# Kernel optimization log

Measured on AMD Instinct MI355X. Metric: run time of the kernel, lower is better.

## Reference

```python
import jax, jax.numpy as jnp
import numpy as np

B, C, H, W = 4, 256, 64, 64
C8, C2 = C // 8, C // 2


def _conv(x, w, b):
    # NCHW conv with SAME padding
    y = jax.lax.conv_general_dilated(x, w, (1, 1), 'SAME',
                                     dimension_numbers=('NCHW', 'OIHW', 'NCHW'))
    return y + b[None, :, None, None]


def _bn(x, s, bi, m, v):
    # eval-mode batchnorm, eps matches torch default 1e-5
    inv = jax.lax.rsqrt(v + 1e-5)
    return (x - m[None, :, None, None]) * (inv * s)[None, :, None, None] + bi[None, :, None, None]


def setup_inputs() -> dict:
    ks = jax.random.split(jax.random.key(0), 8)
    return {
        'x': jax.random.normal(ks[0], (B, C, H, W), jnp.float32),
        'q_w': jax.random.normal(ks[1], (C8, C, 3, 3), jnp.float32) * 0.02,
        'q_b': jnp.zeros((C8,), jnp.float32),
        'q_bn_s': jnp.ones((C8,), jnp.float32),
        'q_bn_b': jnp.zeros((C8,), jnp.float32),
        'q_bn_m': jnp.zeros((C8,), jnp.float32),
        'q_bn_v': jnp.ones((C8,), jnp.float32),
        'k_w': jax.random.normal(ks[2], (C8, C, 3, 3), jnp.float32) * 0.02,
        'k_b': jnp.zeros((C8,), jnp.float32),
        'k_bn_s': jnp.ones((C8,), jnp.float32),
        'k_bn_b': jnp.zeros((C8,), jnp.float32),
        'k_bn_m': jnp.zeros((C8,), jnp.float32),
        'k_bn_v': jnp.ones((C8,), jnp.float32),
        'v_w': jax.random.normal(ks[3], (C, C), jnp.float32) * 0.02,
        'v_b': jnp.zeros((C,), jnp.float32),
        'gamma': jnp.full((1,), 0.5, jnp.float32),
        'c_w1': jax.random.normal(ks[4], (C2, C), jnp.float32) * 0.02,
        'c_b1': jnp.zeros((C2,), jnp.float32),
        'c_w2': jax.random.normal(ks[5], (C, C2), jnp.float32) * 0.02,
        'c_b2': jnp.zeros((C,), jnp.float32),
        's_vw': jax.random.normal(ks[6], (C, C), jnp.float32) * 0.02,
        's_vb': jnp.zeros((C,), jnp.float32),
        's_cw': jax.random.normal(ks[7], (1, 2, 3, 3), jnp.float32) * 0.1,
        's_cb': jnp.zeros((1,), jnp.float32),
        's_bn_s': jnp.ones((1,), jnp.float32),
        's_bn_b': jnp.zeros((1,), jnp.float32),
        's_bn_m': jnp.zeros((1,), jnp.float32),
        's_bn_v': jnp.ones((1,), jnp.float32),
    }


def reference(x, q_w, q_b, q_bn_s, q_bn_b, q_bn_m, q_bn_v,
              k_w, k_b, k_bn_s, k_bn_b, k_bn_m, k_bn_v,
              v_w, v_b, gamma, c_w1, c_b1, c_w2, c_b2,
              s_vw, s_vb, s_cw, s_cb, s_bn_s, s_bn_b, s_bn_m, s_bn_v):
    Bn, Cn, Hn, Wn = x.shape
    HW = Hn * Wn

    # ---- SelfAttention branch ----
    q = jax.nn.relu(_bn(_conv(x, q_w, q_b), q_bn_s, q_bn_b, q_bn_m, q_bn_v)).reshape(Bn, -1, HW)  # [B,C8,HW]
    k = jax.nn.relu(_bn(_conv(x, k_w, k_b), k_bn_s, k_bn_b, k_bn_m, k_bn_v)).reshape(Bn, -1, HW)  # [B,C8,HW]
    aff = jax.nn.softmax(jnp.einsum('bcn,bcm->bnm', q, k), axis=-1)  # [B,HW,HW]
    v = (jnp.einsum('bchw,oc->bohw', x, v_w) + v_b[None, :, None, None]).reshape(Bn, Cn, HW)
    wts = jnp.einsum('bcm,bnm->bcn', v, aff).reshape(Bn, Cn, Hn, Wn)
    selfA = gamma * wts + x

    # ---- Channel mean/max attention ----
    def fc(s):  # s: [B,C]
        h = jax.nn.relu(s @ c_w1.T + c_b1)
        return h @ c_w2.T + c_b2

    gate = jax.nn.sigmoid(fc(x.mean((2, 3))) + fc(x.max((2, 3))))  # [B,C]
    channelA = x * gate[:, :, None, None]

    # ---- Spatial mean/max attention ----
    v2 = jnp.einsum('bchw,oc->bohw', x, s_vw) + s_vb[None, :, None, None]  # [B,C,H,W]
    sm = jnp.stack([v2.max(1), v2.mean(1)], axis=1)  # [B,2,H,W]
    a = _bn(_conv(sm, s_cw, s_cb), s_bn_s, s_bn_b, s_bn_m, s_bn_v)  # [B,1,H,W]
    a = jax.nn.softmax(a[:, 0], axis=-1)  # [B,H,W], softmax over W
    spatialA = jnp.einsum('bchw,bwk->bchk', x, a)  # batched matmul, needs H==W

    return selfA + channelA + spatialA
```

## Files before the change

kernel.cpp:

```cpp
#include <hip/hip_runtime.h>
#include <math.h>

#define NB 4
#define NC 256
#define NHW 4096
#define NC8 32
#define NC2 128

typedef unsigned short u16;
typedef __attribute__((ext_vector_type(8))) short s8v;
typedef __attribute__((ext_vector_type(4))) float f4v;

__device__ __forceinline__ u16 f2bf(float x) {
    unsigned int u = __builtin_bit_cast(unsigned int, x);
    u += 0x7FFFu + ((u >> 16) & 1u);
    return (u16)(u >> 16);
}
__device__ __forceinline__ float bf2f(u16 h) {
    unsigned int u = ((unsigned int)h) << 16;
    return __builtin_bit_cast(float, u);
}

#define MFMA16(a, b, c) __builtin_amdgcn_mfma_f32_16x16x32_bf16((a), (b), (c), 0, 0, 0)

__global__ __launch_bounds__(256) void k_conv_qk(
    const float* __restrict__ x,
    const float* __restrict__ qw, const float* __restrict__ kw,
    float* __restrict__ part)
{
    __shared__ float plane[2][64 * 65];
    const int cog = blockIdx.x;
    const int cic = blockIdx.y;
    const int b   = blockIdx.z;
    const int t   = threadIdx.x;
    const int co0 = cog * 4;
    const bool isq = co0 < NC8;
    const int oc0 = isq ? co0 : co0 - NC8;
    const float* wsel = isq ? qw : kw;
    const int ci0 = cic * 64;
    const int r  = t >> 2;
    const int c0 = (t & 3) * 16;
    float acc[4][16];
#pragma unroll
    for (int j = 0; j < 4; ++j)
#pragma unroll
        for (int q = 0; q < 16; ++q) acc[j][q] = 0.f;

    const float* xb = x + (size_t)b * NC * NHW;
    float4 pf[4];
    {
        const float4* src = (const float4*)(xb + (size_t)ci0 * NHW);
#pragma unroll
        for (int u = 0; u < 4; ++u) pf[u] = src[t + 256 * u];
    }
    for (int ci = ci0; ci < ci0 + 64; ++ci) {
        const int cur = ci & 1;
#pragma unroll
        for (int u = 0; u < 4; ++u) {
            int g  = (t + 256 * u) << 2;
            int rr = g >> 6, cc = g & 63;
            float* p = &plane[cur][rr * 65 + cc];
            p[0] = pf[u].x; p[1] = pf[u].y; p[2] = pf[u].z; p[3] = pf[u].w;
        }
        __syncthreads();
        if (ci + 1 < ci0 + 64) {
            const float4* src = (const float4*)(xb + (size_t)(ci + 1) * NHW);
#pragma unroll
            for (int u = 0; u < 4; ++u) pf[u] = src[t + 256 * u];
        }
        float w9[4][9];
#pragma unroll
        for (int j = 0; j < 4; ++j)
#pragma unroll
            for (int u = 0; u < 9; ++u)
                w9[j][u] = wsel[((size_t)(oc0 + j) * NC + ci) * 9 + u];
#pragma unroll
        for (int dy = 0; dy < 3; ++dy) {
            int rr = r + dy - 1;
            if (rr >= 0 && rr <= 63) {
                const float* row = &plane[cur][rr * 65];
                float tv[18];
#pragma unroll
                for (int jj = 0; jj < 18; ++jj) {
                    int cc = c0 + jj - 1;
                    tv[jj] = (cc >= 0 && cc < 64) ? row[cc] : 0.f;
                }
#pragma unroll
                for (int j = 0; j < 4; ++j) {
                    float wa = w9[j][dy * 3 + 0], wb = w9[j][dy * 3 + 1], wc = w9[j][dy * 3 + 2];
#pragma unroll
                    for (int q = 0; q < 16; ++q)
                        acc[j][q] += wa * tv[q] + wb * tv[q + 1] + wc * tv[q + 2];
                }
            }
        }
        __syncthreads();
    }
    float* pp = part + (((size_t)(cic * 4 + b) * 64 + co0) * NHW) + r * 64 + c0;
#pragma unroll
    for (int j = 0; j < 4; ++j)
#pragma unroll
        for (int q4 = 0; q4 < 4; ++q4) {
            float4 o;
            o.x = acc[j][q4 * 4 + 0]; o.y = acc[j][q4 * 4 + 1];
            o.z = acc[j][q4 * 4 + 2]; o.w = acc[j][q4 * 4 + 3];
            *(float4*)(pp + (size_t)j * NHW + q4 * 4) = o;
        }
}

__global__ __launch_bounds__(256) void k_qk_finish(
    const float* __restrict__ part,
    const float* __restrict__ qb, const float* __restrict__ qbs, const float* __restrict__ qbb,
    const float* __restrict__ qbm, const float* __restrict__ qbv,
    const float* __restrict__ kb, const float* __restrict__ kbs, const float* __restrict__ kbb,
    const float* __restrict__ kbm, const float* __restrict__ kbv,
    u16* __restrict__ qh, u16* __restrict__ ql,
    u16* __restrict__ kh, u16* __restrict__ kl)
{
    const int t = threadIdx.x;
    const int b = blockIdx.y;
    const int n = blockIdx.x * 64 + (t & 63);
    const int coq = t >> 6;
    const int cb2 = coq * 16;
    float s[16];
#pragma unroll
    for (int j = 0; j < 16; ++j) s[j] = 0.f;
#pragma unroll
    for (int cic = 0; cic < 4; ++cic)
#pragma unroll
        for (int j = 0; j < 16; ++j)
            s[j] += part[(((size_t)(cic * 4 + b)) * 64 + cb2 + j) * NHW + n];
    const bool isq = coq < 2;
    u16 hi[16], lo[16];
#pragma unroll
    for (int j = 0; j < 16; ++j) {
        int oc = (coq & 1) * 16 + j;
        float cbv = isq ? qb[oc]  : kb[oc];
        float sv  = isq ? qbs[oc] : kbs[oc];
        float bbv = isq ? qbb[oc] : kbb[oc];
        float mv  = isq ? qbm[oc] : kbm[oc];
        float vv  = isq ? qbv[oc] : kbv[oc];
        float inv = rsqrtf(vv + 1e-5f);
        float scale = inv * sv;
        float shift = (cbv - mv) * scale + bbv;
        float y = fmaxf(s[j] * scale + shift, 0.f);
        hi[j] = f2bf(y);
        lo[j] = f2bf(y - bf2f(hi[j]));
    }
    u16* dh = isq ? qh : kh;
    u16* dl = isq ? ql : kl;
    size_t base = ((size_t)b * NHW + n) * 32 + (coq & 1) * 16;
    uint4 ph0, ph1, pl0, pl1;
    ph0.x = (unsigned)hi[0]  | ((unsigned)hi[1]  << 16);
    ph0.y = (unsigned)hi[2]  | ((unsigned)hi[3]  << 16);
    ph0.z = (unsigned)hi[4]  | ((unsigned)hi[5]  << 16);
    ph0.w = (unsigned)hi[6]  | ((unsigned)hi[7]  << 16);
    ph1.x = (unsigned)hi[8]  | ((unsigned)hi[9]  << 16);
    ph1.y = (unsigned)hi[10] | ((unsigned)hi[11] << 16);
    ph1.z = (unsigned)hi[12] | ((unsigned)hi[13] << 16);
    ph1.w = (unsigned)hi[14] | ((unsigned)hi[15] << 16);
    pl0.x = (unsigned)lo[0]  | ((unsigned)lo[1]  << 16);
    pl0.y = (unsigned)lo[2]  | ((unsigned)lo[3]  << 16);
    pl0.z = (unsigned)lo[4]  | ((unsigned)lo[5]  << 16);
    pl0.w = (unsigned)lo[6]  | ((unsigned)lo[7]  << 16);
    pl1.x = (unsigned)lo[8]  | ((unsigned)lo[9]  << 16);
    pl1.y = (unsigned)lo[10] | ((unsigned)lo[11] << 16);
    pl1.z = (unsigned)lo[12] | ((unsigned)lo[13] << 16);
    pl1.w = (unsigned)lo[14] | ((unsigned)lo[15] << 16);
    *(uint4*)&dh[base]     = ph0;
    *(uint4*)&dh[base + 8] = ph1;
    *(uint4*)&dl[base]     = pl0;
    *(uint4*)&dl[base + 8] = pl1;
}

__global__ __launch_bounds__(256) void k_gemm_vv2(
    const float* __restrict__ x,
    const float* __restrict__ vw, const float* __restrict__ vb,
    const float* __restrict__ sw, const float* __restrict__ sb,
    float* __restrict__ v2T, u16* __restrict__ vhi, u16* __restrict__ vlo)
{
    __shared__ float Ax[16 * 68];
    __shared__ float Bw1[16 * 68];
    __shared__ float Bw2[16 * 68];
    const int t  = threadIdx.x;
    const int n0 = blockIdx.x * 64;
    const int o0 = blockIdx.y * 64;
    const int b  = blockIdx.z;
    const int ni = t & 15, oi = t >> 4;
    float a1[4][4], a2[4][4];
#pragma unroll
    for (int i = 0; i < 4; ++i)
#pragma unroll
        for (int j = 0; j < 4; ++j) { a1[i][j] = 0.f; a2[i][j] = 0.f; }

    const int sk  = t >> 4;
    const int sf  = t & 15;
    const int so  = t & 63;
    const int skq = t >> 6;
    const float* xb = x + ((size_t)b * NC) * NHW + n0;

    float4 ax = *(const float4*)(xb + (size_t)sk * NHW + sf * 4);
    float4 f1 = *(const float4*)(vw + (size_t)(o0 + so) * NC + skq * 4);
    float4 f2 = *(const float4*)(sw + (size_t)(o0 + so) * NC + skq * 4);

    for (int c0 = 0; c0 < NC; c0 += 16) {
        *(float4*)&Ax[sk * 68 + sf * 4] = ax;
        Bw1[(skq * 4 + 0) * 68 + so] = f1.x;
        Bw1[(skq * 4 + 1) * 68 + so] = f1.y;
        Bw1[(skq * 4 + 2) * 68 + so] = f1.z;
        Bw1[(skq * 4 + 3) * 68 + so] = f1.w;
        Bw2[(skq * 4 + 0) * 68 + so] = f2.x;
        Bw2[(skq * 4 + 1) * 68 + so] = f2.y;
        Bw2[(skq * 4 + 2) * 68 + so] = f2.z;
        Bw2[(skq * 4 + 3) * 68 + so] = f2.w;
        __syncthreads();
        if (c0 + 16 < NC) {
            ax = *(const float4*)(xb + (size_t)(c0 + 16 + sk) * NHW + sf * 4);
            f1 = *(const float4*)(vw + (size_t)(o0 + so) * NC + c0 + 16 + skq * 4);
            f2 = *(const float4*)(sw + (size_t)(o0 + so) * NC + c0 + 16 + skq * 4);
        }
#pragma unroll
        for (int k = 0; k < 16; ++k) {
            float4 af = *(const float4*)&Ax[k * 68 + ni * 4];
            float4 g1 = *(const float4*)&Bw1[k * 68 + oi * 4];
            float4 g2 = *(const float4*)&Bw2[k * 68 + oi * 4];
            const float* ap = (const float*)&af;
            const float* p1 = (const float*)&g1;
            const float* p2 = (const float*)&g2;
#pragma unroll
            for (int i = 0; i < 4; ++i)
#pragma unroll
                for (int j = 0; j < 4; ++j) {
                    a1[i][j] += ap[i] * p1[j];
                    a2[i][j] += ap[i] * p2[j];
                }
        }
        __syncthreads();
    }
    float vb4[4], sb4[4];
#pragma unroll
    for (int j = 0; j < 4; ++j) { vb4[j] = vb[o0 + oi * 4 + j]; sb4[j] = sb[o0 + oi * 4 + j]; }
#pragma unroll
    for (int i = 0; i < 4; ++i) {
        size_t idx = ((size_t)b * NHW + n0 + ni * 4 + i) * NC + o0 + oi * 4;
        float4 o2v;
        o2v.x = a2[i][0] + sb4[0]; o2v.y = a2[i][1] + sb4[1];
        o2v.z = a2[i][2] + sb4[2]; o2v.w = a2[i][3] + sb4[3];
        *(float4*)&v2T[idx] = o2v;
    }
#pragma unroll
    for (int j = 0; j < 4; ++j) {
        u16 h[4], l[4];
#pragma unroll
        for (int i = 0; i < 4; ++i) {
            float y = a1[i][j] + vb4[j];
            h[i] = f2bf(y);
            l[i] = f2bf(y - bf2f(h[i]));
        }
        size_t vi = ((size_t)b * NC + o0 + oi * 4 + j) * NHW + n0 + ni * 4;
        uint2 uh, ul;
        uh.x = (unsigned)h[0] | ((unsigned)h[1] << 16);
        uh.y = (unsigned)h[2] | ((unsigned)h[3] << 16);
        ul.x = (unsigned)l[0] | ((unsigned)l[1] << 16);
        ul.y = (unsigned)l[2] | ((unsigned)l[3] << 16);
        *(uint2*)&vhi[vi] = uh;
        *(uint2*)&vlo[vi] = ul;
    }
}

__global__ __launch_bounds__(256) void k_reduce_v2(const float* __restrict__ v2T,
                                                   float* __restrict__ smo)
{
    const int t = threadIdx.x;
    const int lane = t & 63, wv = t >> 6;
    const int row = blockIdx.x * 4 + wv;
    float4 f = ((const float4*)(v2T + (size_t)row * NC))[lane];
    float mx = fmaxf(fmaxf(f.x, f.y), fmaxf(f.z, f.w));
    float sm = f.x + f.y + f.z + f.w;
#pragma unroll
    for (int off = 32; off; off >>= 1) {
        mx = fmaxf(mx, __shfl_down(mx, off));
        sm += __shfl_down(sm, off);
    }
    if (lane == 0) {
        int b = row >> 12, n = row & 4095;
        smo[((size_t)b * 2 + 0) * NHW + n] = mx;
        smo[((size_t)b * 2 + 1) * NHW + n] = sm * (1.f / NC);
    }
}

__global__ __launch_bounds__(256) void k_spatial(
    const float* __restrict__ smo, const float* __restrict__ scw,
    const float* __restrict__ scb, const float* __restrict__ sbs,
    const float* __restrict__ sbb2, const float* __restrict__ sbm,
    const float* __restrict__ sbv, float* __restrict__ Amat)
{
    __shared__ float ch[2][64 * 68];
    __shared__ float lg[64 * 68];
    const int t = threadIdx.x;
    const int b = blockIdx.x;
#pragma unroll
    for (int u = 0; u < 8; ++u) {
        int g  = t + 256 * u;
        int c  = g >> 10, gi = g & 1023;
        int row = gi >> 4, col4 = (gi & 15) * 4;
        float4 f = ((const float4*)(smo + ((size_t)b * 2 + c) * NHW))[gi];
        *(float4*)&ch[c][row * 68 + col4] = f;
    }
    __syncthreads();
    float w9[2][9];
#pragma unroll
    for (int ic = 0; ic < 2; ++ic)
#pragma unroll
        for (int j = 0; j < 9; ++j) w9[ic][j] = scw[ic * 9 + j];
    float A0, Bsh;
    {
        float inv = rsqrtf(sbv[0] + 1e-5f);
        A0  = inv * sbs[0];
        Bsh = (scb[0] - sbm[0]) * A0 + sbb2[0];
    }
#pragma unroll
    for (int u = 0; u < 16; ++u) {
        int px = t + 256 * u;
        int h = px >> 6, w = px & 63;
        float acc = 0.f;
#pragma unroll
        for (int ic = 0; ic < 2; ++ic)
#pragma unroll
            for (int dy = 0; dy < 3; ++dy) {
                int rr = h + dy - 1;
                if (rr < 0 || rr > 63) continue;
#pragma unroll
                for (int dx = 0; dx < 3; ++dx) {
                    int cc = w + dx - 1;
                    if (cc < 0 || cc > 63) continue;
                    acc += w9[ic][dy * 3 + dx] * ch[ic][rr * 68 + cc];
                }
            }
        lg[h * 68 + w] = acc * A0 + Bsh;
    }
    __syncthreads();
    if (t < 64) {
        float M = -INFINITY;
        for (int k2 = 0; k2 < 64; ++k2) M = fmaxf(M, lg[t * 68 + k2]);
        float L = 0.f;
        for (int k2 = 0; k2 < 64; ++k2) L += __expf(lg[t * 68 + k2] - M);
        float rli = 1.f / L;
        for (int k2 = 0; k2 < 64; ++k2)
            Amat[(size_t)b * NHW + t * 64 + k2] = __expf(lg[t * 68 + k2] - M) * rli;
    }
}

__global__ __launch_bounds__(256) void k_xstats(const float* __restrict__ x,
                                                float* __restrict__ smean,
                                                float* __restrict__ smax)
{
    const int t = threadIdx.x;
    const int c = blockIdx.x, b = blockIdx.y;
    const float* row = x + ((size_t)b * NC + c) * NHW;
    float s = 0.f, m = -INFINITY;
#pragma unroll
    for (int u = 0; u < 4; ++u) {
        float4 f = ((const float4*)row)[t + 256 * u];
        s += f.x + f.y + f.z + f.w;
        m = fmaxf(m, fmaxf(fmaxf(f.x, f.y), fmaxf(f.z, f.w)));
    }
    __shared__ float red[8];
    const int lane = t & 63, wv = t >> 6;
#pragma unroll
    for (int off = 32; off; off >>= 1) {
        s += __shfl_down(s, off);
        m = fmaxf(m, __shfl_down(m, off));
    }
    if (lane == 0) { red[wv] = s; red[4 + wv] = m; }
    __syncthreads();
    if (t == 0) {
        float S = red[0] + red[1] + red[2] + red[3];
        float M = fmaxf(fmaxf(red[4], red[5]), fmaxf(red[6], red[7]));
        smean[b * NC + c] = S * (1.f / NHW);
        smax[b * NC + c]  = M;
    }
}

__global__ __launch_bounds__(256) void k_gate(
    const float* __restrict__ smean, const float* __restrict__ smax,
    const float* __restrict__ w1, const float* __restrict__ b1,
    const float* __restrict__ w2, const float* __restrict__ b2,
    float* __restrict__ gate)
{
    __shared__ float smL[256], sxL[256], hL[256];
    const int t = threadIdx.x;
    const int b = blockIdx.x;
    smL[t] = smean[b * NC + t];
    sxL[t] = smax[b * NC + t];
    __syncthreads();
    {
        const int j = t & 127;
        const float* in = (t < 128) ? smL : sxL;
        const float* wr = w1 + (size_t)j * NC;
        float acc = b1[j];
        for (int c = 0; c < NC; c += 4) {
            float4 f = *(const float4*)(wr + c);
            acc += f.x * in[c] + f.y * in[c + 1] + f.z * in[c + 2] + f.w * in[c + 3];
        }
        hL[t] = fmaxf(acc, 0.f);
    }
    __syncthreads();
    {
        const float* wr = w2 + (size_t)t * NC2;
        float acc = 2.f * b2[t];
        for (int j = 0; j < NC2; j += 4) {
            float4 f = *(const float4*)(wr + j);
            acc += f.x * (hL[j]     + hL[128 + j])
                 + f.y * (hL[j + 1] + hL[129 + j])
                 + f.z * (hL[j + 2] + hL[130 + j])
                 + f.w * (hL[j + 3] + hL[131 + j]);
        }
        gate[b * NC + t] = 1.f / (1.f + __expf(-acc));
    }
}

__global__ __launch_bounds__(64) void k_softstats(
    const u16* __restrict__ qh, const u16* __restrict__ ql,
    const u16* __restrict__ kh, const u16* __restrict__ kl,
    float* __restrict__ mx, float* __restrict__ rl)
{
    const int t  = threadIdx.x;
    const int li = t & 15, g = t >> 4;
    const int n0 = blockIdx.x * 16;
    const int b  = blockIdx.y;
    const size_t qoff = ((size_t)b * NHW + n0 + li) * 32 + g * 8;
    const s8v qfh = *(const s8v*)&qh[qoff];
    const s8v qfl = *(const s8v*)&ql[qoff];
    const size_t kb0 = ((size_t)b * NHW + li) * 32 + g * 8;
    s8v ka0 = *(const s8v*)&kh[kb0];
    s8v ka1 = *(const s8v*)&kh[kb0 + 512];
    s8v la0 = *(const s8v*)&kl[kb0];
    s8v la1 = *(const s8v*)&kl[kb0 + 512];
    float mrun = -INFINITY, lrun = 0.f;
    for (int it = 0; it < 128; ++it) {
        f4v c0 = {0.f, 0.f, 0.f, 0.f}, c1 = {0.f, 0.f, 0.f, 0.f};
        c0 = MFMA16(ka0, qfh, c0); c0 = MFMA16(ka0, qfl, c0); c0 = MFMA16(la0, qfh, c0);
        c1 = MFMA16(ka1, qfh, c1); c1 = MFMA16(ka1, qfl, c1); c1 = MFMA16(la1, qfh, c1);
        if (it + 1 < 128) {
            size_t o = kb0 + (size_t)(it + 1) * 1024;
            ka0 = *(const s8v*)&kh[o];
            ka1 = *(const s8v*)&kh[o + 512];
            la0 = *(const s8v*)&kl[o];
            la1 = *(const s8v*)&kl[o + 512];
        }
        float tmax = fmaxf(fmaxf(fmaxf(c0[0], c0[1]), fmaxf(c0[2], c0[3])),
                           fmaxf(fmaxf(c1[0], c1[1]), fmaxf(c1[2], c1[3])));
        tmax = fmaxf(tmax, __shfl_xor(tmax, 16));
        tmax = fmaxf(tmax, __shfl_xor(tmax, 32));
        float nm = fmaxf(mrun, tmax);
        float ls = 0.f;
#pragma unroll
        for (int r = 0; r < 4; ++r) ls += __expf(c0[r] - nm);
#pragma unroll
        for (int r = 0; r < 4; ++r) ls += __expf(c1[r] - nm);
        ls += __shfl_xor(ls, 16);
        ls += __shfl_xor(ls, 32);
        lrun = lrun * __expf(mrun - nm) + ls;
        mrun = nm;
    }
    if (g == 0) {
        mx[(size_t)b * NHW + n0 + li] = mrun;
        rl[(size_t)b * NHW + n0 + li] = 1.f / lrun;
    }
}

__global__ __launch_bounds__(256, 2) void k_flash(
    const u16* __restrict__ qh, const u16* __restrict__ ql,
    const u16* __restrict__ kh, const u16* __restrict__ kl,
    const u16* __restrict__ vhi, const u16* __restrict__ vlo,
    const float* __restrict__ mx, const float* __restrict__ rl,
    float* __restrict__ w0, float* __restrict__ w1)
{
    __shared__ __align__(16) u16 SvH[256 * 40];
    __shared__ __align__(16) u16 SvL[256 * 40];
    __shared__ __align__(16) u16 Sp[4][2][16 * 40];
    const int t = threadIdx.x;
    const int bid = blockIdx.x;
    const int v   = (bid & 7) * 64 + (bid >> 3);
    const int n0  = (v & 63) * 64;
    const int mh  = (v >> 6) & 1;
    const int b   = v >> 7;
    const int mbase = mh * 2048;
    const int li = t & 15, g = (t >> 4) & 3, wv = t >> 6;
    const int sc = t >> 2, sp = t & 3;
    const size_t qoff = ((size_t)b * NHW + n0 + wv * 16 + li) * 32 + g * 8;
    const s8v qfh = *(const s8v*)&qh[qoff];
    const s8v qfl = *(const s8v*)&ql[qoff];
    const float mxv = mx[(size_t)b * NHW + n0 + wv * 16 + li];
    const float rlv = rl[(size_t)b * NHW + n0 + wv * 16 + li];
    f4v acc[16];
#pragma unroll
    for (int nt = 0; nt < 16; ++nt) { f4v z = {0.f, 0.f, 0.f, 0.f}; acc[nt] = z; }
    size_t vr[4];
#pragma unroll
    for (int u = 0; u < 4; ++u)
        vr[u] = ((size_t)b * NC + sc + u * 64) * NHW + mbase;
    s8v pvh[4], pvl[4];
#pragma unroll
    for (int u = 0; u < 4; ++u) {
        pvh[u] = *(const s8v*)&vhi[vr[u] + sp * 8];
        pvl[u] = *(const s8v*)&vlo[vr[u] + sp * 8];
    }
    const size_t kb0 = ((size_t)b * NHW + mbase + li) * 32 + g * 8;
    s8v ka0 = *(const s8v*)&kh[kb0];
    s8v ka1 = *(const s8v*)&kh[kb0 + 512];
    s8v la0 = *(const s8v*)&kl[kb0];
    s8v la1 = *(const s8v*)&kl[kb0 + 512];

    for (int it = 0; it < 64; ++it) {
        __syncthreads();
#pragma unroll
        for (int u = 0; u < 4; ++u) {
            *(s8v*)&SvH[(sc + u * 64) * 40 + sp * 8] = pvh[u];
            *(s8v*)&SvL[(sc + u * 64) * 40 + sp * 8] = pvl[u];
        }
        __syncthreads();
        if (it + 1 < 64) {
#pragma unroll
            for (int u = 0; u < 4; ++u) {
                pvh[u] = *(const s8v*)&vhi[vr[u] + (size_t)(it + 1) * 32 + sp * 8];
                pvl[u] = *(const s8v*)&vlo[vr[u] + (size_t)(it + 1) * 32 + sp * 8];
            }
        }
        f4v c0 = {0.f, 0.f, 0.f, 0.f}, c1 = {0.f, 0.f, 0.f, 0.f};
        c0 = MFMA16(ka0, qfh, c0); c0 = MFMA16(ka0, qfl, c0); c0 = MFMA16(la0, qfh, c0);
        c1 = MFMA16(ka1, qfh, c1); c1 = MFMA16(ka1, qfl, c1); c1 = MFMA16(la1, qfh, c1);
        if (it + 1 < 64) {
            size_t o = kb0 + (size_t)(it + 1) * 1024;
            ka0 = *(const s8v*)&kh[o];
            ka1 = *(const s8v*)&kh[o + 512];
            la0 = *(const s8v*)&kl[o];
            la1 = *(const s8v*)&kl[o + 512];
        }
        u16 h0[4], l0[4], h1[4], l1[4];
#pragma unroll
        for (int r = 0; r < 4; ++r) {
            float p = __expf(c0[r] - mxv) * rlv;
            h0[r] = f2bf(p); l0[r] = f2bf(p - bf2f(h0[r]));
            float q = __expf(c1[r] - mxv) * rlv;
            h1[r] = f2bf(q); l1[r] = f2bf(q - bf2f(h1[r]));
        }
        uint2 uw;
        uw.x = (unsigned)h0[0] | ((unsigned)h0[1] << 16);
        uw.y = (unsigned)h0[2] | ((unsigned)h0[3] << 16);
        *(uint2*)&Sp[wv][0][li * 40 + g * 4] = uw;
        uw.x = (unsigned)h1[0] | ((unsigned)h1[1] << 16);
        uw.y = (unsigned)h1[2] | ((unsigned)h1[3] << 16);
        *(uint2*)&Sp[wv][0][li * 40 + 16 + g * 4] = uw;
        uw.x = (unsigned)l0[0] | ((unsigned)l0[1] << 16);
        uw.y = (unsigned)l0[2] | ((unsigned)l0[3] << 16);
        *(uint2*)&Sp[wv][1][li * 40 + g * 4] = uw;
        uw.x = (unsigned)l1[0] | ((unsigned)l1[1] << 16);
        uw.y = (unsigned)l1[2] | ((unsigned)l1[3] << 16);
        *(uint2*)&Sp[wv][1][li * 40 + 16 + g * 4] = uw;
        s8v ah = *(const s8v*)&Sp[wv][0][li * 40 + g * 8];
        s8v al = *(const s8v*)&Sp[wv][1][li * 40 + g * 8];
#pragma unroll
        for (int nt = 0; nt < 16; ++nt) {
            s8v vh = *(const s8v*)&SvH[(nt * 16 + li) * 40 + g * 8];
            s8v vl = *(const s8v*)&SvL[(nt * 16 + li) * 40 + g * 8];
            acc[nt] = MFMA16(ah, vh, acc[nt]);
            acc[nt] = MFMA16(ah, vl, acc[nt]);
            acc[nt] = MFMA16(al, vh, acc[nt]);
        }
    }
    float* wout = (mh == 0) ? w0 : w1;
#pragma unroll
    for (int nt = 0; nt < 16; ++nt)
#pragma unroll
        for (int r = 0; r < 4; ++r)
            wout[((size_t)b * NHW + n0 + wv * 16 + g * 4 + r) * NC + nt * 16 + li] = acc[nt][r];
}

__global__ __launch_bounds__(256) void k_final(
    const float* __restrict__ x, const float* __restrict__ w0,
    const float* __restrict__ w1, const float* __restrict__ gate,
    const float* __restrict__ Amat, const float* __restrict__ gamma,
    float* __restrict__ out)
{
    const int t = threadIdx.x;
    const int h = blockIdx.x, b = blockIdx.y;
    const int kx = t & 63, wv = t >> 6;
    const float g0 = gamma[0];
    float Areg[64];
#pragma unroll
    for (int w = 0; w < 64; ++w)
        Areg[w] = Amat[(size_t)b * NHW + w * 64 + kx];
    for (int cc = 0; cc < 64; ++cc) {
        const int c = cc * 4 + wv;
        const size_t xidx = ((size_t)(b * NC + c)) * NHW + h * 64 + kx;
        const float xv = x[xidx];
        float spat = 0.f;
#pragma unroll
        for (int w = 0; w < 64; ++w)
            spat += __shfl(xv, w, 64) * Areg[w];
        const size_t widx = ((size_t)b * NHW + h * 64 + kx) * NC + c;
        const float wsum = w0[widx] + w1[widx];
        const float gt = gate[b * NC + c];
        out[xidx] = g0 * wsum + xv * (1.f + gt) + spat;
    }
}

extern "C" void kernel_launch(void* const* d_in, const int* in_sizes, int n_in,
                              void* d_out, int out_size, void* d_ws, size_t ws_size,
                              hipStream_t stream)
{
    const float* x    = (const float*)d_in[0];
    const float* qw   = (const float*)d_in[1];
    const float* qb   = (const float*)d_in[2];
    const float* qbs  = (const float*)d_in[3];
    const float* qbb  = (const float*)d_in[4];
    const float* qbm  = (const float*)d_in[5];
    const float* qbv  = (const float*)d_in[6];
    const float* kw   = (const float*)d_in[7];
    const float* kb   = (const float*)d_in[8];
    const float* kbs  = (const float*)d_in[9];
    const float* kbb  = (const float*)d_in[10];
    const float* kbm  = (const float*)d_in[11];
    const float* kbv  = (const float*)d_in[12];
    const float* vw   = (const float*)d_in[13];
    const float* vb   = (const float*)d_in[14];
    const float* gm   = (const float*)d_in[15];
    const float* cw1  = (const float*)d_in[16];
    const float* cb1  = (const float*)d_in[17];
    const float* cw2  = (const float*)d_in[18];
    const float* cb2  = (const float*)d_in[19];
    const float* svw  = (const float*)d_in[20];
    const float* svb  = (const float*)d_in[21];
    const float* scw  = (const float*)d_in[22];
    const float* scb  = (const float*)d_in[23];
    const float* sbs  = (const float*)d_in[24];
    const float* sbb  = (const float*)d_in[25];
    const float* sbm  = (const float*)d_in[26];
    const float* sbv  = (const float*)d_in[27];

    float* ws    = (float*)d_ws;
    float* part  = ws;
    float* w0    = ws;
    float* v2T   = ws + 4194304;
    float* w1    = ws + 4194304;
    u16*   vhi   = (u16*)(ws + 8388608);
    u16*   vlo   = (u16*)(ws + 10485760);
    u16*   qhB   = (u16*)(ws + 12582912);
    u16*   qlB   = (u16*)(ws + 12845056);
    u16*   khB   = (u16*)(ws + 13107200);
    u16*   klB   = (u16*)(ws + 13369344);
    float* mxp   = ws + 13631488;
    float* rlp   = ws + 13647872;
    float* smean = ws + 13664256;
    float* smax  = ws + 13665280;
    float* gate  = ws + 13666304;
    float* smo   = ws + 13667328;
    float* Amat  = ws + 13700096;

    k_conv_qk  <<<dim3(16, 4, NB), 256, 0, stream>>>(x, qw, kw, part);
    k_qk_finish<<<dim3(64, NB),    256, 0, stream>>>(part, qb, qbs, qbb, qbm, qbv,
                                                     kb, kbs, kbb, kbm, kbv,
                                                     qhB, qlB, khB, klB);
    k_gemm_vv2 <<<dim3(64, 4, NB), 256, 0, stream>>>(x, vw, vb, svw, svb, v2T, vhi, vlo);
    k_reduce_v2<<<dim3(4096),      256, 0, stream>>>(v2T, smo);
    k_spatial  <<<dim3(NB),        256, 0, stream>>>(smo, scw, scb, sbs, sbb, sbm, sbv, Amat);
    k_xstats   <<<dim3(NC, NB),    256, 0, stream>>>(x, smean, smax);
    k_gate     <<<dim3(NB),        256, 0, stream>>>(smean, smax, cw1, cb1, cw2, cb2, gate);
    k_softstats<<<dim3(256, NB),   64,  0, stream>>>(qhB, qlB, khB, klB, mxp, rlp);
    k_flash    <<<dim3(512),       256, 0, stream>>>(qhB, qlB, khB, klB, vhi, vlo,
                                                     mxp, rlp, w0, w1);
    k_final    <<<dim3(64, NB),    256, 0, stream>>>(x, w0, w1, gate, Amat, gm,
                                                     (float*)d_out);
}
```

Baseline: 593.4 us.

## Keep V fragments in registers in flash kernel and tile final spatial matmul

```diff
diff --git a/kernel.cpp b/kernel.cpp
--- a/kernel.cpp
+++ b/kernel.cpp
@@ -9,6 +9,7 @@
 
 typedef unsigned short u16;
 typedef __attribute__((ext_vector_type(8))) short s8v;
+typedef __attribute__((ext_vector_type(4))) short s4v;
 typedef __attribute__((ext_vector_type(4))) float f4v;
 
 __device__ __forceinline__ u16 f2bf(float x) {
@@ -19,6 +20,11 @@
 __device__ __forceinline__ float bf2f(u16 h) {
     unsigned int u = ((unsigned int)h) << 16;
     return __builtin_bit_cast(float, u);
+}
+__device__ __forceinline__ s8v ld_sp(const u16* p) {
+    s4v a = *(const s4v*)p;
+    s4v b = *(const s4v*)(p + 4);
+    return __builtin_shufflevector(a, b, 0, 1, 2, 3, 4, 5, 6, 7);
 }
 
 #define MFMA16(a, b, c) __builtin_amdgcn_mfma_f32_16x16x32_bf16((a), (b), (c), 0, 0, 0)
@@ -477,9 +483,7 @@
     const float* __restrict__ mx, const float* __restrict__ rl,
     float* __restrict__ w0, float* __restrict__ w1)
 {
-    __shared__ __align__(16) u16 SvH[256 * 40];
-    __shared__ __align__(16) u16 SvL[256 * 40];
-    __shared__ __align__(16) u16 Sp[4][2][16 * 40];
+    __shared__ __align__(16) u16 Sp[2][4][16 * 36];
     const int t = threadIdx.x;
     const int bid = blockIdx.x;
     const int v   = (bid & 7) * 64 + (bid >> 3);
@@ -488,94 +492,92 @@
     const int b   = v >> 7;
     const int mbase = mh * 2048;
     const int li = t & 15, g = (t >> 4) & 3, wv = t >> 6;
-    const int sc = t >> 2, sp = t & 3;
+
     const size_t qoff = ((size_t)b * NHW + n0 + wv * 16 + li) * 32 + g * 8;
     const s8v qfh = *(const s8v*)&qh[qoff];
     const s8v qfl = *(const s8v*)&ql[qoff];
     const float mxv = mx[(size_t)b * NHW + n0 + wv * 16 + li];
     const float rlv = rl[(size_t)b * NHW + n0 + wv * 16 + li];
-    f4v acc[16];
-#pragma unroll
-    for (int nt = 0; nt < 16; ++nt) { f4v z = {0.f, 0.f, 0.f, 0.f}; acc[nt] = z; }
-    size_t vr[4];
-#pragma unroll
-    for (int u = 0; u < 4; ++u)
-        vr[u] = ((size_t)b * NC + sc + u * 64) * NHW + mbase;
-    s8v pvh[4], pvl[4];
-#pragma unroll
-    for (int u = 0; u < 4; ++u) {
-        pvh[u] = *(const s8v*)&vhi[vr[u] + sp * 8];
-        pvl[u] = *(const s8v*)&vlo[vr[u] + sp * 8];
-    }
+
+    f4v acc[4][4];
+#pragma unroll
+    for (int i = 0; i < 4; ++i)
+#pragma unroll
+        for (int j = 0; j < 4; ++j) { f4v z = {0.f, 0.f, 0.f, 0.f}; acc[i][j] = z; }
+
     const size_t kb0 = ((size_t)b * NHW + mbase + li) * 32 + g * 8;
     s8v ka0 = *(const s8v*)&kh[kb0];
     s8v ka1 = *(const s8v*)&kh[kb0 + 512];
     s8v la0 = *(const s8v*)&kl[kb0];
     s8v la1 = *(const s8v*)&kl[kb0 + 512];
 
+    const size_t vb0 = ((size_t)b * NC + wv * 64 + li) * NHW + mbase + g * 8;
+    s8v vfh[4], vfl[4];
+#pragma unroll
+    for (int ct = 0; ct < 4; ++ct) {
+        vfh[ct] = *(const s8v*)&vhi[vb0 + (size_t)ct * 16 * NHW];
+        vfl[ct] = *(const s8v*)&vlo[vb0 + (size_t)ct * 16 * NHW];
+    }
+
     for (int it = 0; it < 64; ++it) {
-        __syncthreads();
-#pragma unroll
-        for (int u = 0; u < 4; ++u) {
-            *(s8v*)&SvH[(sc + u * 64) * 40 + sp * 8] = pvh[u];
-            *(s8v*)&SvL[(sc + u * 64) * 40 + sp * 8] = pvl[u];
-        }
-        __syncthreads();
-        if (it + 1 < 64) {
-#pragma unroll
-            for (int u = 0; u < 4; ++u) {
-                pvh[u] = *(const s8v*)&vhi[vr[u] + (size_t)(it + 1) * 32 + sp * 8];
-                pvl[u] = *(const s8v*)&vlo[vr[u] + (size_t)(it + 1) * 32 + sp * 8];
-            }
-        }
         f4v c0 = {0.f, 0.f, 0.f, 0.f}, c1 = {0.f, 0.f, 0.f, 0.f};
         c0 = MFMA16(ka0, qfh, c0); c0 = MFMA16(ka0, qfl, c0); c0 = MFMA16(la0, qfh, c0);
         c1 = MFMA16(ka1, qfh, c1); c1 = MFMA16(ka1, qfl, c1); c1 = MFMA16(la1, qfh, c1);
-        if (it + 1 < 64) {
+        {
             size_t o = kb0 + (size_t)(it + 1) * 1024;
             ka0 = *(const s8v*)&kh[o];
             ka1 = *(const s8v*)&kh[o + 512];
             la0 = *(const s8v*)&kl[o];
             la1 = *(const s8v*)&kl[o + 512];
         }
-        u16 h0[4], l0[4], h1[4], l1[4];
+        u16 h0[4], h1[4];
 #pragma unroll
         for (int r = 0; r < 4; ++r) {
-            float p = __expf(c0[r] - mxv) * rlv;
-            h0[r] = f2bf(p); l0[r] = f2bf(p - bf2f(h0[r]));
-            float q = __expf(c1[r] - mxv) * rlv;
-            h1[r] = f2bf(q); l1[r] = f2bf(q - bf2f(h1[r]));
-        }
-        uint2 uw;
-        uw.x = (unsigned)h0[0] | ((unsigned)h0[1] << 16);
-        uw.y = (unsigned)h0[2] | ((unsigned)h0[3] << 16);
-        *(uint2*)&Sp[wv][0][li * 40 + g * 4] = uw;
-        uw.x = (unsigned)h1[0] | ((unsigned)h1[1] << 16);
-        uw.y = (unsigned)h1[2] | ((unsigned)h1[3] << 16);
-        *(uint2*)&Sp[wv][0][li * 40 + 16 + g * 4] = uw;
-        uw.x = (unsigned)l0[0] | ((unsigned)l0[1] << 16);
-        uw.y = (unsigned)l0[2] | ((unsigned)l0[3] << 16);
-        *(uint2*)&Sp[wv][1][li * 40 + g * 4] = uw;
-        uw.x = (unsigned)l1[0] | ((unsigned)l1[1] << 16);
-        uw.y = (unsigned)l1[2] | ((unsigned)l1[3] << 16);
-        *(uint2*)&Sp[wv][1][li * 40 + 16 + g * 4] = uw;
-        s8v ah = *(const s8v*)&Sp[wv][0][li * 40 + g * 8];
-        s8v al = *(const s8v*)&Sp[wv][1][li * 40 + g * 8];
-#pragma unroll
-        for (int nt = 0; nt < 16; ++nt) {
-            s8v vh = *(const s8v*)&SvH[(nt * 16 + li) * 40 + g * 8];
-            s8v vl = *(const s8v*)&SvL[(nt * 16 + li) * 40 + g * 8];
-            acc[nt] = MFMA16(ah, vh, acc[nt]);
-            acc[nt] = MFMA16(ah, vl, acc[nt]);
-            acc[nt] = MFMA16(al, vh, acc[nt]);
+            h0[r] = f2bf(__expf(c0[r] - mxv) * rlv);
+            h1[r] = f2bf(__expf(c1[r] - mxv) * rlv);
+        }
+        u16* sp = &Sp[it & 1][wv][0];
+        uint2 uw0, uw1;
+        uw0.x = (unsigned)h0[0] | ((unsigned)h0[1] << 16);
+        uw0.y = (unsigned)h0[2] | ((unsigned)h0[3] << 16);
+        uw1.x = (unsigned)h1[0] | ((unsigned)h1[1] << 16);
+        uw1.y = (unsigned)h1[2] | ((unsigned)h1[3] << 16);
+        *(uint2*)&sp[li * 36 + g * 4]      = uw0;
+        *(uint2*)&sp[li * 36 + 16 + g * 4] = uw1;
+        __syncthreads();
+        s8v pa0 = ld_sp(&Sp[it & 1][0][li * 36 + g * 8]);
+        s8v pa1 = ld_sp(&Sp[it & 1][1][li * 36 + g * 8]);
+        s8v pa2 = ld_sp(&Sp[it & 1][2][li * 36 + g * 8]);
+        s8v pa3 = ld_sp(&Sp[it & 1][3][li * 36 + g * 8]);
+#pragma unroll
+        for (int ct = 0; ct < 4; ++ct) {
+            acc[0][ct] = MFMA16(pa0, vfh[ct], acc[0][ct]);
+            acc[0][ct] = MFMA16(pa0, vfl[ct], acc[0][ct]);
+            acc[1][ct] = MFMA16(pa1, vfh[ct], acc[1][ct]);
+            acc[1][ct] = MFMA16(pa1, vfl[ct], acc[1][ct]);
+            acc[2][ct] = MFMA16(pa2, vfh[ct], acc[2][ct]);
+            acc[2][ct] = MFMA16(pa2, vfl[ct], acc[2][ct]);
+            acc[3][ct] = MFMA16(pa3, vfh[ct], acc[3][ct]);
+            acc[3][ct] = MFMA16(pa3, vfl[ct], acc[3][ct]);
+        }
+        {
+            size_t o = vb0 + (size_t)(it + 1) * 32;
+#pragma unroll
+            for (int ct = 0; ct < 4; ++ct) {
+                vfh[ct] = *(const s8v*)&vhi[o + (size_t)ct * 16 * NHW];
+                vfl[ct] = *(const s8v*)&vlo[o + (size_t)ct * 16 * NHW];
+            }
         }
     }
     float* wout = (mh == 0) ? w0 : w1;
 #pragma unroll
-    for (int nt = 0; nt < 16; ++nt)
-#pragma unroll
-        for (int r = 0; r < 4; ++r)
-            wout[((size_t)b * NHW + n0 + wv * 16 + g * 4 + r) * NC + nt * 16 + li] = acc[nt][r];
+    for (int ng = 0; ng < 4; ++ng)
+#pragma unroll
+        for (int ct = 0; ct < 4; ++ct)
+#pragma unroll
+            for (int r = 0; r < 4; ++r)
+                wout[((size_t)b * NHW + n0 + ng * 16 + g * 4 + r) * NC
+                     + wv * 64 + ct * 16 + li] = acc[ng][ct][r];
 }
 
 __global__ __launch_bounds__(256) void k_final(
@@ -584,26 +586,63 @@
     const float* __restrict__ Amat, const float* __restrict__ gamma,
     float* __restrict__ out)
 {
+    __shared__ float As[64 * 65];
+    __shared__ float xs[64 * 65];
     const int t = threadIdx.x;
     const int h = blockIdx.x, b = blockIdx.y;
-    const int kx = t & 63, wv = t >> 6;
     const float g0 = gamma[0];
-    float Areg[64];
-#pragma unroll
-    for (int w = 0; w < 64; ++w)
-        Areg[w] = Amat[(size_t)b * NHW + w * 64 + kx];
-    for (int cc = 0; cc < 64; ++cc) {
-        const int c = cc * 4 + wv;
-        const size_t xidx = ((size_t)(b * NC + c)) * NHW + h * 64 + kx;
-        const float xv = x[xidx];
-        float spat = 0.f;
-#pragma unroll
-        for (int w = 0; w < 64; ++w)
-            spat += __shfl(xv, w, 64) * Areg[w];
-        const size_t widx = ((size_t)b * NHW + h * 64 + kx) * NC + c;
-        const float wsum = w0[widx] + w1[widx];
-        const float gt = gate[b * NC + c];
-        out[xidx] = g0 * wsum + xv * (1.f + gt) + spat;
+    const int kq = t >> 4;
+    const int cq = t & 15;
+#pragma unroll
+    for (int u = 0; u < 4; ++u) {
+        int gidx = t + 256 * u;
+        int w = gidx >> 4, k4 = (gidx & 15) * 4;
+        float4 f = ((const float4*)(Amat + (size_t)b * NHW))[gidx];
+        *(float4*)&As[w * 65 + k4] = f;
+    }
+    for (int ch = 0; ch < 4; ++ch) {
+        __syncthreads();
+#pragma unroll
+        for (int u = 0; u < 4; ++u) {
+            int gidx = t + 256 * u;
+            int c = gidx >> 4, w4 = (gidx & 15) * 4;
+            float4 f = *(const float4*)(x + ((size_t)(b * NC) + ch * 64 + c) * NHW + h * 64 + w4);
+            xs[(w4 + 0) * 65 + c] = f.x;
+            xs[(w4 + 1) * 65 + c] = f.y;
+            xs[(w4 + 2) * 65 + c] = f.z;
+            xs[(w4 + 3) * 65 + c] = f.w;
+        }
+        __syncthreads();
+        float acc[4][4];
+#pragma unroll
+        for (int i = 0; i < 4; ++i)
+#pragma unroll
+            for (int j = 0; j < 4; ++j) acc[i][j] = 0.f;
+        for (int w = 0; w < 64; ++w) {
+            float4 av = *(const float4*)&As[w * 65 + kq * 4];
+            float4 xv = *(const float4*)&xs[w * 65 + cq * 4];
+            const float* ap = (const float*)&av;
+            const float* xp = (const float*)&xv;
+#pragma unroll
+            for (int i = 0; i < 4; ++i)
+#pragma unroll
+                for (int j = 0; j < 4; ++j)
+                    acc[i][j] += xp[i] * ap[j];
+        }
+#pragma unroll
+        for (int i = 0; i < 4; ++i) {
+            const int c = ch * 64 + cq * 4 + i;
+            const float gt1 = 1.f + gate[b * NC + c];
+#pragma unroll
+            for (int j = 0; j < 4; ++j) {
+                const int k = kq * 4 + j;
+                const int n = h * 64 + k;
+                const float xv = xs[k * 65 + cq * 4 + i];
+                const size_t widx = ((size_t)b * NHW + n) * NC + c;
+                const float wsum = w0[widx] + w1[widx];
+                out[((size_t)(b * NC + c)) * NHW + n] = g0 * wsum + xv * gt1 + acc[i][j];
+            }
+        }
     }
 }
 
```

After: 533.3 us. 1.11x faster.
